# Kernel tuning notes

Hardware: AMD Instinct MI355X
Metric: run time of the kernel (lower is better)

The kernel has to match this reference:

```python
import jax, jax.numpy as jnp
import numpy as np

T, H, I, E, K = 1024, 1024, 512, 32, 4   # tokens, hidden, moe_inter, n_experts, top_k
G, TG, NS = 8, 4, 2                      # n_group, topk_group, n_shared_experts
C = 2 * T * K // E                       # expert capacity (no-drop headroom)
SCALE = 2.5                              # routed_scaling_factor


def setup_inputs() -> dict:
    key = jax.random.key(0)
    ks = jax.random.split(key, 7)
    s = 0.02
    return dict(
        hidden_states=jax.random.normal(ks[0], (T, H), jnp.float32),
        gate_w=jax.random.normal(ks[1], (E, H), jnp.float32) * s,
        e_bias=jax.random.normal(ks[2], (E,), jnp.float32) * 0.1,
        w_gate_up=jax.random.normal(ks[3], (E, 2 * I, H), jnp.float32) * s,
        w_down=jax.random.normal(ks[4], (E, H, I), jnp.float32) * s,
        w_gate_up_shared=jax.random.normal(ks[5], (2 * I * NS, H), jnp.float32) * s,
        w_down_shared=jax.random.normal(ks[6], (H, I * NS), jnp.float32) * s,
    )


def reference(hidden_states, gate_w, e_bias, w_gate_up, w_down, w_gate_up_shared, w_down_shared):
    x = hidden_states                                   # (T, H)
    # --- gate + sigmoid scoring (noaux_tc) ---
    logits = x @ gate_w.T                               # (T, E)
    scores = jax.nn.sigmoid(logits.astype(jnp.float32))
    sfc = scores + e_bias                               # scores_for_choice
    # --- group-limited top-k: top-2 sum per group, keep topk_group groups ---
    group_scores = jax.lax.top_k(sfc.reshape(T, G, E // G), 2)[0].sum(-1)  # (T, G)
    grp_idx = jax.lax.top_k(group_scores, TG)[1]        # (T, TG)
    gmask = jnp.zeros((T, G), jnp.float32).at[jnp.arange(T)[:, None], grp_idx].set(1.0)
    smask = jnp.repeat(gmask, E // G, axis=1)           # (T, E)
    sfc_m = jnp.where(smask > 0, sfc, 0.0)
    topk_idx = jax.lax.top_k(sfc_m, K)[1]               # (T, K)
    tw = jnp.take_along_axis(scores, topk_idx, axis=1)  # weights from raw scores
    tw = tw / (tw.sum(-1, keepdims=True) + 1e-20)       # norm_topk_prob
    tw = tw * SCALE
    # --- capacity-based dispatch (position within expert via cumsum of one-hot) ---
    e_flat = topk_idx.reshape(-1)                       # (T*K,)
    oh = jax.nn.one_hot(e_flat, E, dtype=jnp.float32)   # (T*K, E)
    pos = jnp.sum((jnp.cumsum(oh, axis=0) - 1.0) * oh, axis=-1).astype(jnp.int32)
    keep = (pos < C).astype(jnp.float32)                # capacity sized to never drop
    pos_c = jnp.clip(pos, 0, C - 1)
    t_flat = jnp.repeat(jnp.arange(T), K)
    combine = jnp.zeros((T, E, C), jnp.float32).at[t_flat, e_flat, pos_c].add(tw.reshape(-1) * keep)
    dispatch = jnp.zeros((T, E, C), jnp.float32).at[t_flat, e_flat, pos_c].add(keep)
    # --- grouped expert MLP (gate_up -> SiluAndMul -> down) ---
    xe = jnp.einsum('tec,th->ech', dispatch, x)         # (E, C, H)
    gu = jnp.einsum('ech,eoh->eco', xe, w_gate_up)      # (E, C, 2I)
    act = jax.nn.silu(gu[..., :I]) * gu[..., I:]
    ye = jnp.einsum('eci,ehi->ech', act, w_down)        # (E, C, H)
    routed = jnp.einsum('tec,ech->th', combine, ye)     # (T, H)
    # --- shared experts MLP on residual ---
    IS = I * NS
    gus = x @ w_gate_up_shared.T                        # (T, 2*IS)
    acts = jax.nn.silu(gus[:, :IS]) * gus[:, IS:]
    shared = acts @ w_down_shared.T                     # (T, H)
    return routed + shared
```

## Files before the change

### kernel.cpp

```cpp
#include <hip/hip_runtime.h>
#include <hip/hip_bf16.h>
#include <math.h>

#define T_TOK 1024
#define H_DIM 1024
#define I_DIM 512
#define E_NUM 32
#define K_TOP 4
#define G_NUM 8
#define TG_NUM 4
#define CAP 256
#define IS_DIM 1024
#define RSCALE 2.5f

#define WS_EIDX_OFF   1024
#define WS_WN_OFF     17408
#define WS_STOK_OFF   33792
#define WS_SW_OFF     66560
#define WS_ACT_OFF    99328
#define WS_ACTS_OFF   (99328 + (size_t)E_NUM*CAP*I_DIM*2)

typedef __attribute__((ext_vector_type(8))) short short8v;
typedef __attribute__((ext_vector_type(4))) short short4v;
typedef __attribute__((ext_vector_type(4))) float f32x4;

__device__ __forceinline__ short f2bf(float f) {
    unsigned u = __float_as_uint(f);
    u += 0x7FFFu + ((u >> 16) & 1u);
    return (short)(u >> 16);
}
__device__ __forceinline__ float silu_(float g) { return g / (1.f + expf(-g)); }

#define LDSTRIDE 40

__global__ __launch_bounds__(256) void gate_kernel(
    const float* __restrict__ x, const float* __restrict__ gate_w,
    const float* __restrict__ e_bias,
    int* __restrict__ eidx, float* __restrict__ wnorm)
{
    __shared__ float xs[H_DIM];
    __shared__ float logits[E_NUM];
    const int t = blockIdx.x;
    const int tid = threadIdx.x;
    ((float4*)xs)[tid] = ((const float4*)(x + (size_t)t * H_DIM))[tid];
    __syncthreads();

    const int e = tid >> 3, sub = tid & 7;
    const float* gw = gate_w + (size_t)e * H_DIM + sub * 128;
    const float* xr = xs + sub * 128;
    float p = 0.f;
    #pragma unroll 8
    for (int h = 0; h < 128; ++h) p += xr[h] * gw[h];
    for (int off = 4; off; off >>= 1) p += __shfl_down(p, off, 8);
    if (sub == 0) logits[e] = p;
    __syncthreads();
    if (tid != 0) return;

    float sc[E_NUM], sfc[E_NUM];
    for (int i = 0; i < E_NUM; ++i) {
        sc[i] = 1.f / (1.f + expf(-logits[i]));
        sfc[i] = sc[i] + e_bias[i];
    }
    float gs[G_NUM];
    for (int g = 0; g < G_NUM; ++g) {
        float m1 = -1e30f, m2 = -1e30f;
        for (int j = 0; j < E_NUM / G_NUM; ++j) {
            float v = sfc[g * (E_NUM / G_NUM) + j];
            if (v > m1) { m2 = m1; m1 = v; } else if (v > m2) m2 = v;
        }
        gs[g] = m1 + m2;
    }
    bool gm[G_NUM];
    for (int g = 0; g < G_NUM; ++g) gm[g] = false;
    for (int it = 0; it < TG_NUM; ++it) {
        int best = -1; float bv = -1e30f;
        for (int g = 0; g < G_NUM; ++g) if (!gm[g] && gs[g] > bv) { bv = gs[g]; best = g; }
        gm[best] = true;
    }
    float sm[E_NUM];
    for (int i = 0; i < E_NUM; ++i) sm[i] = gm[i / (E_NUM / G_NUM)] ? sfc[i] : 0.0f;
    int idx[K_TOP]; float w[K_TOP]; float tsum = 0.f;
    for (int it = 0; it < K_TOP; ++it) {
        int best = 0; float bv = -1e30f;
        for (int i = 0; i < E_NUM; ++i) if (sm[i] > bv) { bv = sm[i]; best = i; }
        sm[best] = -1e30f;
        idx[it] = best; w[it] = sc[best]; tsum += w[it];
    }
    float inv = RSCALE / (tsum + 1e-20f);
    const int base = t * K_TOP;
    for (int it = 0; it < K_TOP; ++it) {
        eidx[base + it] = idx[it];
        wnorm[base + it] = w[it] * inv;
    }
}

__global__ __launch_bounds__(256) void assign_kernel(
    const int* __restrict__ eidx, const float* __restrict__ wnorm,
    int* __restrict__ cnt, int* __restrict__ slot_token, float* __restrict__ slot_w)
{
    __shared__ int   se[T_TOK * K_TOP];
    __shared__ float swt[T_TOK * K_TOP];
    const int tid = threadIdx.x;
    for (int i = tid; i < T_TOK * K_TOP; i += 256) { se[i] = eidx[i]; swt[i] = wnorm[i]; }
    __syncthreads();

    const int e = tid >> 3;
    const int seg = tid & 7;
    const int base = seg * 512;
    int c = 0;
    for (int i = 0; i < 512; ++i) c += (se[base + i] == e);
    int excl = 0, total = 0;
    for (int s = 0; s < 8; ++s) {
        int cs = __shfl(c, s, 8);
        total += cs;
        if (s < seg) excl += cs;
    }
    if (seg == 0) cnt[e] = total;
    int pos = excl;
    for (int i = 0; i < 512; ++i) {
        if (se[base + i] == e) {
            if (pos < CAP) {
                slot_token[e * CAP + pos] = (base + i) >> 2;
                slot_w[e * CAP + pos] = swt[base + i];
            }
            ++pos;
        }
    }
}

#define WAVE_SETUP() \
    const int tid = threadIdx.x; const int lane = tid & 63; const int wid = tid >> 6; \
    const int wm = wid & 1, wn = wid >> 1; \
    const int lr16 = lane & 15, kc = lane >> 4; \
    const int kq = tid & 7; const int rbase = tid >> 3;

#define DECL_ACC() f32x4 acc[4][4]; \
    _Pragma("unroll") for (int i_ = 0; i_ < 4; ++i_) \
    _Pragma("unroll") for (int j_ = 0; j_ < 4; ++j_) acc[i_][j_] = 0.f;

#define STAGE_F32(dstoff, src, valid) do { \
    float4 v_ = (valid) ? *(const float4*)(src) : make_float4(0.f,0.f,0.f,0.f); \
    short4v sv_; sv_.x = f2bf(v_.x); sv_.y = f2bf(v_.y); sv_.z = f2bf(v_.z); sv_.w = f2bf(v_.w); \
    *(short4v*)(dstoff) = sv_; } while (0)

#define COMPUTE32() do { \
    short8v a_[4], b_[4]; \
    _Pragma("unroll") for (int mt = 0; mt < 4; ++mt) \
        a_[mt] = *(const short8v*)&As[(wm*64 + mt*16 + lr16)*LDSTRIDE + kc*8]; \
    _Pragma("unroll") for (int nt = 0; nt < 4; ++nt) \
        b_[nt] = *(const short8v*)&Bs[(wn*64 + nt*16 + lr16)*LDSTRIDE + kc*8]; \
    _Pragma("unroll") for (int mt = 0; mt < 4; ++mt) \
    _Pragma("unroll") for (int nt = 0; nt < 4; ++nt) \
        acc[mt][nt] = __builtin_amdgcn_mfma_f32_16x16x32_bf16(a_[mt], b_[nt], acc[mt][nt], 0, 0, 0); \
} while (0)

__global__ __launch_bounds__(256) void moe_gu_kernel(
    const float* __restrict__ x, const float* __restrict__ w_gate_up,
    const int* __restrict__ cnt, const int* __restrict__ slot_token,
    const float* __restrict__ slot_w, short* __restrict__ act)
{
    const int e = blockIdx.z;
    const int ne = min(cnt[e], CAP);
    const int r0 = blockIdx.y * 128;
    if (r0 >= ne) return;
    const int nI0 = blockIdx.x * 64;

    __shared__ __align__(16) short As[128 * LDSTRIDE];
    __shared__ __align__(16) short Bs[128 * LDSTRIDE];
    __shared__ int   toks[128];
    __shared__ float sws[128];

    WAVE_SETUP();
    if (tid < 128) {
        int p = r0 + tid;
        toks[tid] = (p < ne) ? slot_token[e * CAP + p] : 0;
        sws[tid]  = (p < ne) ? slot_w[e * CAP + p] : 0.f;
    }
    __syncthreads();

    const float* aptr[4]; bool aval[4]; int aoff[4];
    const float* bptr[4]; int boff[4];
    const float* wgu_e = w_gate_up + (size_t)e * (2 * I_DIM) * H_DIM;
    #pragma unroll
    for (int i = 0; i < 4; ++i) {
        int r = rbase + i * 32;
        aval[i] = (r0 + r) < ne;
        aptr[i] = x + (size_t)toks[r] * H_DIM + kq * 4;
        aoff[i] = r * LDSTRIDE + kq * 4;
        int c = r;
        int wrow = ((c >> 4) & 1) * I_DIM + nI0 + (c >> 5) * 16 + (c & 15);
        bptr[i] = wgu_e + (size_t)wrow * H_DIM + kq * 4;
        boff[i] = aoff[i];
    }

    DECL_ACC();
    for (int k0 = 0; k0 < H_DIM; k0 += 32) {
        #pragma unroll
        for (int i = 0; i < 4; ++i) STAGE_F32(&As[aoff[i]], aptr[i] + k0, aval[i]);
        #pragma unroll
        for (int i = 0; i < 4; ++i) STAGE_F32(&Bs[boff[i]], bptr[i] + k0, true);
        __syncthreads();
        COMPUTE32();
        __syncthreads();
    }

    #pragma unroll
    for (int mt = 0; mt < 4; ++mt) {
        #pragma unroll
        for (int q = 0; q < 2; ++q) {
            f32x4 g = acc[mt][2 * q], u = acc[mt][2 * q + 1];
            int colI = nI0 + (wn * 2 + q) * 16 + lr16;
            #pragma unroll
            for (int i = 0; i < 4; ++i) {
                int rl = wm * 64 + mt * 16 + kc * 4 + i;
                int p = r0 + rl;
                if (p < ne) {
                    float s = sws[rl];
                    float v = s * silu_(g[i]) * u[i];
                    act[((size_t)e * CAP + p) * I_DIM + colI] = f2bf(v);
                }
            }
        }
    }
}

__global__ __launch_bounds__(256) void moe_down_kernel(
    const short* __restrict__ act, const float* __restrict__ w_down,
    const int* __restrict__ cnt, const int* __restrict__ slot_token,
    float* __restrict__ out)
{
    const int e = blockIdx.z;
    const int ne = min(cnt[e], CAP);
    const int r0 = blockIdx.y * 128;
    if (r0 >= ne) return;
    const int h0 = blockIdx.x * 128;

    __shared__ __align__(16) short As[128 * LDSTRIDE];
    __shared__ __align__(16) short Bs[128 * LDSTRIDE];
    __shared__ int toks[128];

    WAVE_SETUP();
    if (tid < 128) {
        int p = r0 + tid;
        toks[tid] = (p < ne) ? slot_token[e * CAP + p] : 0;
    }
    __syncthreads();

    const short* aptr[4]; bool aval[4]; int aoff[4];
    const float* bptr[4];
    const float* wd_e = w_down + (size_t)e * H_DIM * I_DIM;
    #pragma unroll
    for (int i = 0; i < 4; ++i) {
        int r = rbase + i * 32;
        aval[i] = (r0 + r) < ne;
        aptr[i] = act + ((size_t)e * CAP + r0 + r) * I_DIM + kq * 4;
        aoff[i] = r * LDSTRIDE + kq * 4;
        bptr[i] = wd_e + (size_t)(h0 + r) * I_DIM + kq * 4;
    }

    DECL_ACC();
    for (int k0 = 0; k0 < I_DIM; k0 += 32) {
        #pragma unroll
        for (int i = 0; i < 4; ++i) {
            short4v sv = aval[i] ? *(const short4v*)(aptr[i] + k0) : (short4v)(short)0;
            *(short4v*)&As[aoff[i]] = sv;
        }
        #pragma unroll
        for (int i = 0; i < 4; ++i) STAGE_F32(&Bs[aoff[i]], bptr[i] + k0, true);
        __syncthreads();
        COMPUTE32();
        __syncthreads();
    }

    #pragma unroll
    for (int mt = 0; mt < 4; ++mt) {
        #pragma unroll
        for (int i = 0; i < 4; ++i) {
            int rl = wm * 64 + mt * 16 + kc * 4 + i;
            int p = r0 + rl;
            if (p < ne) {
                int tt = toks[rl];
                float* orow = out + (size_t)tt * H_DIM + h0 + wn * 64;
                #pragma unroll
                for (int nt = 0; nt < 4; ++nt)
                    atomicAdd(&orow[nt * 16 + lr16], acc[mt][nt][i]);
            }
        }
    }
}

__global__ __launch_bounds__(256) void shared_gu_kernel(
    const float* __restrict__ x, const float* __restrict__ w_gus,
    short* __restrict__ acts)
{
    const int t0 = blockIdx.y * 128;
    const int nI0 = blockIdx.x * 64;
    __shared__ __align__(16) short As[128 * LDSTRIDE];
    __shared__ __align__(16) short Bs[128 * LDSTRIDE];

    WAVE_SETUP();
    const float* aptr[4]; const float* bptr[4]; int aoff[4];
    #pragma unroll
    for (int i = 0; i < 4; ++i) {
        int r = rbase + i * 32;
        aptr[i] = x + (size_t)(t0 + r) * H_DIM + kq * 4;
        aoff[i] = r * LDSTRIDE + kq * 4;
        int c = r;
        int wrow = ((c >> 4) & 1) * IS_DIM + nI0 + (c >> 5) * 16 + (c & 15);
        bptr[i] = w_gus + (size_t)wrow * H_DIM + kq * 4;
    }

    DECL_ACC();
    for (int k0 = 0; k0 < H_DIM; k0 += 32) {
        #pragma unroll
        for (int i = 0; i < 4; ++i) STAGE_F32(&As[aoff[i]], aptr[i] + k0, true);
        #pragma unroll
        for (int i = 0; i < 4; ++i) STAGE_F32(&Bs[aoff[i]], bptr[i] + k0, true);
        __syncthreads();
        COMPUTE32();
        __syncthreads();
    }

    #pragma unroll
    for (int mt = 0; mt < 4; ++mt) {
        #pragma unroll
        for (int q = 0; q < 2; ++q) {
            f32x4 g = acc[mt][2 * q], u = acc[mt][2 * q + 1];
            int colI = nI0 + (wn * 2 + q) * 16 + lr16;
            #pragma unroll
            for (int i = 0; i < 4; ++i) {
                int t = t0 + wm * 64 + mt * 16 + kc * 4 + i;
                acts[(size_t)t * IS_DIM + colI] = f2bf(silu_(g[i]) * u[i]);
            }
        }
    }
}

__global__ __launch_bounds__(256) void shared_down_kernel(
    const short* __restrict__ acts, const float* __restrict__ w_ds,
    float* __restrict__ out)
{
    const int t0 = blockIdx.y * 128;
    const int h0 = blockIdx.x * 128;
    __shared__ __align__(16) short As[128 * LDSTRIDE];
    __shared__ __align__(16) short Bs[128 * LDSTRIDE];

    WAVE_SETUP();
    const short* aptr[4]; const float* bptr[4]; int aoff[4];
    #pragma unroll
    for (int i = 0; i < 4; ++i) {
        int r = rbase + i * 32;
        aptr[i] = acts + (size_t)(t0 + r) * IS_DIM + kq * 4;
        aoff[i] = r * LDSTRIDE + kq * 4;
        bptr[i] = w_ds + (size_t)(h0 + r) * IS_DIM + kq * 4;
    }

    DECL_ACC();
    for (int k0 = 0; k0 < IS_DIM; k0 += 32) {
        #pragma unroll
        for (int i = 0; i < 4; ++i) {
            short4v sv = *(const short4v*)(aptr[i] + k0);
            *(short4v*)&As[aoff[i]] = sv;
        }
        #pragma unroll
        for (int i = 0; i < 4; ++i) STAGE_F32(&Bs[aoff[i]], bptr[i] + k0, true);
        __syncthreads();
        COMPUTE32();
        __syncthreads();
    }

    #pragma unroll
    for (int mt = 0; mt < 4; ++mt) {
        #pragma unroll
        for (int i = 0; i < 4; ++i) {
            int t = t0 + wm * 64 + mt * 16 + kc * 4 + i;
            float* orow = out + (size_t)t * H_DIM + h0 + wn * 64;
            #pragma unroll
            for (int nt = 0; nt < 4; ++nt)
                orow[nt * 16 + lr16] = acc[mt][nt][i];
        }
    }
}

extern "C" void kernel_launch(void* const* d_in, const int* in_sizes, int n_in,
                              void* d_out, int out_size, void* d_ws, size_t ws_size,
                              hipStream_t stream) {
    const float* x   = (const float*)d_in[0];
    const float* gw  = (const float*)d_in[1];
    const float* eb  = (const float*)d_in[2];
    const float* wgu = (const float*)d_in[3];
    const float* wd  = (const float*)d_in[4];
    const float* wgs = (const float*)d_in[5];
    const float* wds = (const float*)d_in[6];
    float* out = (float*)d_out;
    char* ws = (char*)d_ws;

    int*   cnt   = (int*)(ws + 0);
    int*   eidx  = (int*)(ws + WS_EIDX_OFF);
    float* wnorm = (float*)(ws + WS_WN_OFF);
    int*   stok  = (int*)(ws + WS_STOK_OFF);
    float* sw    = (float*)(ws + WS_SW_OFF);
    short* act   = (short*)(ws + WS_ACT_OFF);
    short* acts  = (short*)(ws + WS_ACTS_OFF);

    gate_kernel<<<T_TOK, 256, 0, stream>>>(x, gw, eb, eidx, wnorm);
    assign_kernel<<<1, 256, 0, stream>>>(eidx, wnorm, cnt, stok, sw);
    shared_gu_kernel<<<dim3(IS_DIM / 64, T_TOK / 128), 256, 0, stream>>>(x, wgs, acts);
    shared_down_kernel<<<dim3(H_DIM / 128, T_TOK / 128), 256, 0, stream>>>(acts, wds, out);
    moe_gu_kernel<<<dim3(I_DIM / 64, CAP / 128, E_NUM), 256, 0, stream>>>(x, wgu, cnt, stok, sw, act);
    moe_down_kernel<<<dim3(H_DIM / 128, CAP / 128, E_NUM), 256, 0, stream>>>(act, wd, cnt, stok, out);
}
```

Baseline: 492.2 us.

## Use compact 64-row expert tile list with register-prefetched k-loop GEMMs

The assign kernel now builds a compact list of (expert, row-offset) tiles of 64 rows. The MoE GEMMs launch over this list instead of a fixed expert×capacity grid, which cuts the blocks that exit early and the padded rows in partly filled tiles. All four GEMM kernels move to 64×128 block tiles with launch_bounds occupancy hints. They also prefetch the next k-slice from global memory into registers while the current one is computed. FP32-to-bf16 conversion is packed with a byte-permute that rounds half-up rather than to nearest even, and the gate dot product is vectorised with float4. Smaller tiles give each block less reuse, and the rounding change shifts numerics slightly.

```diff
diff --git a/kernel.cpp b/kernel.cpp
--- a/kernel.cpp
+++ b/kernel.cpp
@@ -13,21 +13,33 @@
 #define IS_DIM 1024
 #define RSCALE 2.5f
 
-#define WS_EIDX_OFF   1024
-#define WS_WN_OFF     17408
-#define WS_STOK_OFF   33792
-#define WS_SW_OFF     66560
-#define WS_ACT_OFF    99328
-#define WS_ACTS_OFF   (99328 + (size_t)E_NUM*CAP*I_DIM*2)
+#define WS_CNT_OFF    0
+#define WS_NT_OFF     128
+#define WS_TILE_OFF   256
+#define WS_EIDX_OFF   4096
+#define WS_WN_OFF     20480
+#define WS_STOK_OFF   36864
+#define WS_SW_OFF     69632
+#define WS_ACT_OFF    102400
+#define WS_ACTS_OFF   (102400 + (size_t)E_NUM*CAP*I_DIM*2)
 
 typedef __attribute__((ext_vector_type(8))) short short8v;
-typedef __attribute__((ext_vector_type(4))) short short4v;
 typedef __attribute__((ext_vector_type(4))) float f32x4;
+typedef __attribute__((ext_vector_type(4))) unsigned uint4v;
 
 __device__ __forceinline__ short f2bf(float f) {
     unsigned u = __float_as_uint(f);
     u += 0x7FFFu + ((u >> 16) & 1u);
     return (short)(u >> 16);
+}
+__device__ __forceinline__ unsigned pk2bf(float a, float b) {
+    unsigned ua = __float_as_uint(a) + 0x8000u;
+    unsigned ub = __float_as_uint(b) + 0x8000u;
+    return __builtin_amdgcn_perm(ub, ua, 0x07060302);
+}
+__device__ __forceinline__ uint4v pk8bf(float4 lo, float4 hi) {
+    uint4v r; r.x = pk2bf(lo.x, lo.y); r.y = pk2bf(lo.z, lo.w);
+    r.z = pk2bf(hi.x, hi.y); r.w = pk2bf(hi.z, hi.w); return r;
 }
 __device__ __forceinline__ float silu_(float g) { return g / (1.f + expf(-g)); }
 
@@ -46,11 +58,14 @@
     __syncthreads();
 
     const int e = tid >> 3, sub = tid & 7;
-    const float* gw = gate_w + (size_t)e * H_DIM + sub * 128;
-    const float* xr = xs + sub * 128;
+    const float4* gw4 = (const float4*)(gate_w + (size_t)e * H_DIM + sub * 128);
+    const float4* xr4 = (const float4*)(xs + sub * 128);
     float p = 0.f;
-    #pragma unroll 8
-    for (int h = 0; h < 128; ++h) p += xr[h] * gw[h];
+    #pragma unroll
+    for (int h = 0; h < 32; ++h) {
+        float4 a = xr4[h], b = gw4[h];
+        p += a.x * b.x + a.y * b.y + a.z * b.z + a.w * b.w;
+    }
     for (int off = 4; off; off >>= 1) p += __shfl_down(p, off, 8);
     if (sub == 0) logits[e] = p;
     __syncthreads();
@@ -96,10 +111,12 @@
 
 __global__ __launch_bounds__(256) void assign_kernel(
     const int* __restrict__ eidx, const float* __restrict__ wnorm,
-    int* __restrict__ cnt, int* __restrict__ slot_token, float* __restrict__ slot_w)
+    int* __restrict__ cnt, int* __restrict__ slot_token, float* __restrict__ slot_w,
+    int* __restrict__ ntiles, int* __restrict__ tiles)
 {
     __shared__ int   se[T_TOK * K_TOP];
     __shared__ float swt[T_TOK * K_TOP];
+    __shared__ int   scnt[E_NUM];
     const int tid = threadIdx.x;
     for (int i = tid; i < T_TOK * K_TOP; i += 256) { se[i] = eidx[i]; swt[i] = wnorm[i]; }
     __syncthreads();
@@ -115,7 +132,7 @@
         total += cs;
         if (s < seg) excl += cs;
     }
-    if (seg == 0) cnt[e] = total;
+    if (seg == 0) { cnt[e] = total; scnt[e] = total; }
     int pos = excl;
     for (int i = 0; i < 512; ++i) {
         if (se[base + i] == e) {
@@ -126,161 +143,177 @@
             ++pos;
         }
     }
+    __syncthreads();
+    if (tid == 0) {
+        int nt = 0;
+        for (int ee = 0; ee < E_NUM; ++ee) {
+            int n = min(scnt[ee], CAP);
+            for (int r = 0; r < n; r += 64) {
+                tiles[nt * 4] = ee; tiles[nt * 4 + 1] = r; tiles[nt * 4 + 2] = n;
+                ++nt;
+            }
+        }
+        *ntiles = nt;
+    }
 }
 
 #define WAVE_SETUP() \
     const int tid = threadIdx.x; const int lane = tid & 63; const int wid = tid >> 6; \
     const int wm = wid & 1, wn = wid >> 1; \
     const int lr16 = lane & 15, kc = lane >> 4; \
-    const int kq = tid & 7; const int rbase = tid >> 3;
-
-#define DECL_ACC() f32x4 acc[4][4]; \
-    _Pragma("unroll") for (int i_ = 0; i_ < 4; ++i_) \
+    const int sc_ = tid & 3, srow = tid >> 2;
+
+#define DECL_ACC() f32x4 acc[2][4]; \
+    _Pragma("unroll") for (int i_ = 0; i_ < 2; ++i_) \
     _Pragma("unroll") for (int j_ = 0; j_ < 4; ++j_) acc[i_][j_] = 0.f;
 
-#define STAGE_F32(dstoff, src, valid) do { \
-    float4 v_ = (valid) ? *(const float4*)(src) : make_float4(0.f,0.f,0.f,0.f); \
-    short4v sv_; sv_.x = f2bf(v_.x); sv_.y = f2bf(v_.y); sv_.z = f2bf(v_.z); sv_.w = f2bf(v_.w); \
-    *(short4v*)(dstoff) = sv_; } while (0)
-
-#define COMPUTE32() do { \
-    short8v a_[4], b_[4]; \
-    _Pragma("unroll") for (int mt = 0; mt < 4; ++mt) \
-        a_[mt] = *(const short8v*)&As[(wm*64 + mt*16 + lr16)*LDSTRIDE + kc*8]; \
+#define COMPUTE_2x4() do { \
+    short8v a_[2], b_[4]; \
+    _Pragma("unroll") for (int mt = 0; mt < 2; ++mt) \
+        a_[mt] = *(const short8v*)&As[(wm*32 + mt*16 + lr16)*LDSTRIDE + kc*8]; \
     _Pragma("unroll") for (int nt = 0; nt < 4; ++nt) \
         b_[nt] = *(const short8v*)&Bs[(wn*64 + nt*16 + lr16)*LDSTRIDE + kc*8]; \
-    _Pragma("unroll") for (int mt = 0; mt < 4; ++mt) \
+    _Pragma("unroll") for (int mt = 0; mt < 2; ++mt) \
     _Pragma("unroll") for (int nt = 0; nt < 4; ++nt) \
         acc[mt][nt] = __builtin_amdgcn_mfma_f32_16x16x32_bf16(a_[mt], b_[nt], acc[mt][nt], 0, 0, 0); \
 } while (0)
 
-__global__ __launch_bounds__(256) void moe_gu_kernel(
+__global__ __launch_bounds__(256, 4) void moe_gu_kernel(
     const float* __restrict__ x, const float* __restrict__ w_gate_up,
-    const int* __restrict__ cnt, const int* __restrict__ slot_token,
-    const float* __restrict__ slot_w, short* __restrict__ act)
-{
-    const int e = blockIdx.z;
-    const int ne = min(cnt[e], CAP);
-    const int r0 = blockIdx.y * 128;
-    if (r0 >= ne) return;
+    const int* __restrict__ ntiles, const int* __restrict__ tiles,
+    const int* __restrict__ slot_token, const float* __restrict__ slot_w,
+    short* __restrict__ act)
+{
+    if ((int)blockIdx.y >= *ntiles) return;
+    const int e  = tiles[blockIdx.y * 4];
+    const int r0 = tiles[blockIdx.y * 4 + 1];
+    const int ne = tiles[blockIdx.y * 4 + 2];
     const int nI0 = blockIdx.x * 64;
 
-    __shared__ __align__(16) short As[128 * LDSTRIDE];
+    __shared__ __align__(16) short As[64 * LDSTRIDE];
     __shared__ __align__(16) short Bs[128 * LDSTRIDE];
-    __shared__ int   toks[128];
-    __shared__ float sws[128];
+    __shared__ int   toks[64];
+    __shared__ float sws[64];
 
     WAVE_SETUP();
-    if (tid < 128) {
-        int p = r0 + tid;
-        toks[tid] = (p < ne) ? slot_token[e * CAP + p] : 0;
-        sws[tid]  = (p < ne) ? slot_w[e * CAP + p] : 0.f;
-    }
-    __syncthreads();
-
-    const float* aptr[4]; bool aval[4]; int aoff[4];
-    const float* bptr[4]; int boff[4];
+    if (tid < 64) {
+        int p = r0 + tid; bool v = p < ne;
+        toks[tid] = v ? slot_token[e * CAP + p] : 0;
+        sws[tid]  = v ? slot_w[e * CAP + p] : 0.f;
+    }
+    __syncthreads();
+
+    const float* aptr = x + (size_t)toks[srow] * H_DIM + sc_ * 8;
     const float* wgu_e = w_gate_up + (size_t)e * (2 * I_DIM) * H_DIM;
+    const int cB1 = srow + 64;
+    const int wr0 = ((srow >> 4) & 1) * I_DIM + nI0 + ((srow >> 5) << 4) + (srow & 15);
+    const int wr1 = ((cB1 >> 4) & 1) * I_DIM + nI0 + ((cB1 >> 5) << 4) + (cB1 & 15);
+    const float* bptr0 = wgu_e + (size_t)wr0 * H_DIM + sc_ * 8;
+    const float* bptr1 = wgu_e + (size_t)wr1 * H_DIM + sc_ * 8;
+    const int aoff = srow * LDSTRIDE + sc_ * 8;
+    const int boff0 = srow * LDSTRIDE + sc_ * 8;
+    const int boff1 = cB1 * LDSTRIDE + sc_ * 8;
+
+    DECL_ACC();
+    float4 cA0 = *(const float4*)(aptr), cA1 = *(const float4*)(aptr + 4);
+    float4 cB0a = *(const float4*)(bptr0), cB0b = *(const float4*)(bptr0 + 4);
+    float4 cB1a = *(const float4*)(bptr1), cB1b = *(const float4*)(bptr1 + 4);
+
+    for (int k0 = 0; k0 < H_DIM; k0 += 32) {
+        float4 nA0, nA1, nB0a, nB0b, nB1a, nB1b;
+        const int k1 = k0 + 32;
+        if (k1 < H_DIM) {
+            nA0 = *(const float4*)(aptr + k1);  nA1 = *(const float4*)(aptr + k1 + 4);
+            nB0a = *(const float4*)(bptr0 + k1); nB0b = *(const float4*)(bptr0 + k1 + 4);
+            nB1a = *(const float4*)(bptr1 + k1); nB1b = *(const float4*)(bptr1 + k1 + 4);
+        }
+        *(uint4v*)&As[aoff]  = pk8bf(cA0, cA1);
+        *(uint4v*)&Bs[boff0] = pk8bf(cB0a, cB0b);
+        *(uint4v*)&Bs[boff1] = pk8bf(cB1a, cB1b);
+        __syncthreads();
+        COMPUTE_2x4();
+        __syncthreads();
+        cA0 = nA0; cA1 = nA1; cB0a = nB0a; cB0b = nB0b; cB1a = nB1a; cB1b = nB1b;
+    }
+
     #pragma unroll
-    for (int i = 0; i < 4; ++i) {
-        int r = rbase + i * 32;
-        aval[i] = (r0 + r) < ne;
-        aptr[i] = x + (size_t)toks[r] * H_DIM + kq * 4;
-        aoff[i] = r * LDSTRIDE + kq * 4;
-        int c = r;
-        int wrow = ((c >> 4) & 1) * I_DIM + nI0 + (c >> 5) * 16 + (c & 15);
-        bptr[i] = wgu_e + (size_t)wrow * H_DIM + kq * 4;
-        boff[i] = aoff[i];
-    }
-
-    DECL_ACC();
-    for (int k0 = 0; k0 < H_DIM; k0 += 32) {
-        #pragma unroll
-        for (int i = 0; i < 4; ++i) STAGE_F32(&As[aoff[i]], aptr[i] + k0, aval[i]);
-        #pragma unroll
-        for (int i = 0; i < 4; ++i) STAGE_F32(&Bs[boff[i]], bptr[i] + k0, true);
-        __syncthreads();
-        COMPUTE32();
-        __syncthreads();
-    }
-
-    #pragma unroll
-    for (int mt = 0; mt < 4; ++mt) {
+    for (int mt = 0; mt < 2; ++mt) {
         #pragma unroll
         for (int q = 0; q < 2; ++q) {
             f32x4 g = acc[mt][2 * q], u = acc[mt][2 * q + 1];
-            int colI = nI0 + (wn * 2 + q) * 16 + lr16;
+            int colI = nI0 + wn * 32 + q * 16 + lr16;
             #pragma unroll
             for (int i = 0; i < 4; ++i) {
-                int rl = wm * 64 + mt * 16 + kc * 4 + i;
+                int rl = wm * 32 + mt * 16 + kc * 4 + i;
                 int p = r0 + rl;
                 if (p < ne) {
                     float s = sws[rl];
-                    float v = s * silu_(g[i]) * u[i];
-                    act[((size_t)e * CAP + p) * I_DIM + colI] = f2bf(v);
+                    act[((size_t)e * CAP + p) * I_DIM + colI] = f2bf(s * silu_(g[i]) * u[i]);
                 }
             }
         }
     }
 }
 
-__global__ __launch_bounds__(256) void moe_down_kernel(
+__global__ __launch_bounds__(256, 4) void moe_down_kernel(
     const short* __restrict__ act, const float* __restrict__ w_down,
-    const int* __restrict__ cnt, const int* __restrict__ slot_token,
-    float* __restrict__ out)
-{
-    const int e = blockIdx.z;
-    const int ne = min(cnt[e], CAP);
-    const int r0 = blockIdx.y * 128;
-    if (r0 >= ne) return;
+    const int* __restrict__ ntiles, const int* __restrict__ tiles,
+    const int* __restrict__ slot_token, float* __restrict__ out)
+{
+    if ((int)blockIdx.y >= *ntiles) return;
+    const int e  = tiles[blockIdx.y * 4];
+    const int r0 = tiles[blockIdx.y * 4 + 1];
+    const int ne = tiles[blockIdx.y * 4 + 2];
     const int h0 = blockIdx.x * 128;
 
-    __shared__ __align__(16) short As[128 * LDSTRIDE];
+    __shared__ __align__(16) short As[64 * LDSTRIDE];
     __shared__ __align__(16) short Bs[128 * LDSTRIDE];
-    __shared__ int toks[128];
+    __shared__ int toks[64];
 
     WAVE_SETUP();
-    if (tid < 128) {
+    if (tid < 64) {
         int p = r0 + tid;
         toks[tid] = (p < ne) ? slot_token[e * CAP + p] : 0;
     }
     __syncthreads();
 
-    const short* aptr[4]; bool aval[4]; int aoff[4];
-    const float* bptr[4];
+    const short* aptr = act + ((size_t)e * CAP + r0 + srow) * I_DIM + sc_ * 8;
     const float* wd_e = w_down + (size_t)e * H_DIM * I_DIM;
+    const float* bptr0 = wd_e + (size_t)(h0 + srow) * I_DIM + sc_ * 8;
+    const float* bptr1 = wd_e + (size_t)(h0 + srow + 64) * I_DIM + sc_ * 8;
+    const int aoff = srow * LDSTRIDE + sc_ * 8;
+    const int boff1 = (srow + 64) * LDSTRIDE + sc_ * 8;
+
+    DECL_ACC();
+    short8v cA = *(const short8v*)(aptr);
+    float4 cB0a = *(const float4*)(bptr0), cB0b = *(const float4*)(bptr0 + 4);
+    float4 cB1a = *(const float4*)(bptr1), cB1b = *(const float4*)(bptr1 + 4);
+
+    for (int k0 = 0; k0 < I_DIM; k0 += 32) {
+        short8v nA; float4 nB0a, nB0b, nB1a, nB1b;
+        const int k1 = k0 + 32;
+        if (k1 < I_DIM) {
+            nA = *(const short8v*)(aptr + k1);
+            nB0a = *(const float4*)(bptr0 + k1); nB0b = *(const float4*)(bptr0 + k1 + 4);
+            nB1a = *(const float4*)(bptr1 + k1); nB1b = *(const float4*)(bptr1 + k1 + 4);
+        }
+        *(short8v*)&As[aoff] = cA;
+        *(uint4v*)&Bs[aoff]  = pk8bf(cB0a, cB0b);
+        *(uint4v*)&Bs[boff1] = pk8bf(cB1a, cB1b);
+        __syncthreads();
+        COMPUTE_2x4();
+        __syncthreads();
+        cA = nA; cB0a = nB0a; cB0b = nB0b; cB1a = nB1a; cB1b = nB1b;
+    }
+
     #pragma unroll
-    for (int i = 0; i < 4; ++i) {
-        int r = rbase + i * 32;
-        aval[i] = (r0 + r) < ne;
-        aptr[i] = act + ((size_t)e * CAP + r0 + r) * I_DIM + kq * 4;
-        aoff[i] = r * LDSTRIDE + kq * 4;
-        bptr[i] = wd_e + (size_t)(h0 + r) * I_DIM + kq * 4;
-    }
-
-    DECL_ACC();
-    for (int k0 = 0; k0 < I_DIM; k0 += 32) {
+    for (int mt = 0; mt < 2; ++mt) {
         #pragma unroll
         for (int i = 0; i < 4; ++i) {
-            short4v sv = aval[i] ? *(const short4v*)(aptr[i] + k0) : (short4v)(short)0;
-            *(short4v*)&As[aoff[i]] = sv;
-        }
-        #pragma unroll
-        for (int i = 0; i < 4; ++i) STAGE_F32(&Bs[aoff[i]], bptr[i] + k0, true);
-        __syncthreads();
-        COMPUTE32();
-        __syncthreads();
-    }
-
-    #pragma unroll
-    for (int mt = 0; mt < 4; ++mt) {
-        #pragma unroll
-        for (int i = 0; i < 4; ++i) {
-            int rl = wm * 64 + mt * 16 + kc * 4 + i;
+            int rl = wm * 32 + mt * 16 + kc * 4 + i;
             int p = r0 + rl;
             if (p < ne) {
-                int tt = toks[rl];
-                float* orow = out + (size_t)tt * H_DIM + h0 + wn * 64;
+                float* orow = out + (size_t)toks[rl] * H_DIM + h0 + wn * 64;
                 #pragma unroll
                 for (int nt = 0; nt < 4; ++nt)
                     atomicAdd(&orow[nt * 16 + lr16], acc[mt][nt][i]);
@@ -289,91 +322,105 @@
     }
 }
 
-__global__ __launch_bounds__(256) void shared_gu_kernel(
+__global__ __launch_bounds__(256, 4) void shared_gu_kernel(
     const float* __restrict__ x, const float* __restrict__ w_gus,
     short* __restrict__ acts)
 {
-    const int t0 = blockIdx.y * 128;
+    const int t0 = blockIdx.y * 64;
     const int nI0 = blockIdx.x * 64;
-    __shared__ __align__(16) short As[128 * LDSTRIDE];
+    __shared__ __align__(16) short As[64 * LDSTRIDE];
     __shared__ __align__(16) short Bs[128 * LDSTRIDE];
 
     WAVE_SETUP();
-    const float* aptr[4]; const float* bptr[4]; int aoff[4];
+    const float* aptr = x + (size_t)(t0 + srow) * H_DIM + sc_ * 8;
+    const int cB1 = srow + 64;
+    const int wr0 = ((srow >> 4) & 1) * IS_DIM + nI0 + ((srow >> 5) << 4) + (srow & 15);
+    const int wr1 = ((cB1 >> 4) & 1) * IS_DIM + nI0 + ((cB1 >> 5) << 4) + (cB1 & 15);
+    const float* bptr0 = w_gus + (size_t)wr0 * H_DIM + sc_ * 8;
+    const float* bptr1 = w_gus + (size_t)wr1 * H_DIM + sc_ * 8;
+    const int aoff = srow * LDSTRIDE + sc_ * 8;
+    const int boff1 = cB1 * LDSTRIDE + sc_ * 8;
+
+    DECL_ACC();
+    float4 cA0 = *(const float4*)(aptr), cA1 = *(const float4*)(aptr + 4);
+    float4 cB0a = *(const float4*)(bptr0), cB0b = *(const float4*)(bptr0 + 4);
+    float4 cB1a = *(const float4*)(bptr1), cB1b = *(const float4*)(bptr1 + 4);
+
+    for (int k0 = 0; k0 < H_DIM; k0 += 32) {
+        float4 nA0, nA1, nB0a, nB0b, nB1a, nB1b;
+        const int k1 = k0 + 32;
+        if (k1 < H_DIM) {
+            nA0 = *(const float4*)(aptr + k1);  nA1 = *(const float4*)(aptr + k1 + 4);
+            nB0a = *(const float4*)(bptr0 + k1); nB0b = *(const float4*)(bptr0 + k1 + 4);
+            nB1a = *(const float4*)(bptr1 + k1); nB1b = *(const float4*)(bptr1 + k1 + 4);
+        }
+        *(uint4v*)&As[aoff]  = pk8bf(cA0, cA1);
+        *(uint4v*)&Bs[aoff]  = pk8bf(cB0a, cB0b);
+        *(uint4v*)&Bs[boff1] = pk8bf(cB1a, cB1b);
+        __syncthreads();
+        COMPUTE_2x4();
+        __syncthreads();
+        cA0 = nA0; cA1 = nA1; cB0a = nB0a; cB0b = nB0b; cB1a = nB1a; cB1b = nB1b;
+    }
+
     #pragma unroll
-    for (int i = 0; i < 4; ++i) {
-        int r = rbase + i * 32;
-        aptr[i] = x + (size_t)(t0 + r) * H_DIM + kq * 4;
-        aoff[i] = r * LDSTRIDE + kq * 4;
-        int c = r;
-        int wrow = ((c >> 4) & 1) * IS_DIM + nI0 + (c >> 5) * 16 + (c & 15);
-        bptr[i] = w_gus + (size_t)wrow * H_DIM + kq * 4;
-    }
-
-    DECL_ACC();
-    for (int k0 = 0; k0 < H_DIM; k0 += 32) {
-        #pragma unroll
-        for (int i = 0; i < 4; ++i) STAGE_F32(&As[aoff[i]], aptr[i] + k0, true);
-        #pragma unroll
-        for (int i = 0; i < 4; ++i) STAGE_F32(&Bs[aoff[i]], bptr[i] + k0, true);
-        __syncthreads();
-        COMPUTE32();
-        __syncthreads();
-    }
-
-    #pragma unroll
-    for (int mt = 0; mt < 4; ++mt) {
+    for (int mt = 0; mt < 2; ++mt) {
         #pragma unroll
         for (int q = 0; q < 2; ++q) {
             f32x4 g = acc[mt][2 * q], u = acc[mt][2 * q + 1];
-            int colI = nI0 + (wn * 2 + q) * 16 + lr16;
+            int colI = nI0 + wn * 32 + q * 16 + lr16;
             #pragma unroll
             for (int i = 0; i < 4; ++i) {
-                int t = t0 + wm * 64 + mt * 16 + kc * 4 + i;
+                int t = t0 + wm * 32 + mt * 16 + kc * 4 + i;
                 acts[(size_t)t * IS_DIM + colI] = f2bf(silu_(g[i]) * u[i]);
             }
         }
     }
 }
 
-__global__ __launch_bounds__(256) void shared_down_kernel(
+__global__ __launch_bounds__(256, 4) void shared_down_kernel(
     const short* __restrict__ acts, const float* __restrict__ w_ds,
     float* __restrict__ out)
 {
-    const int t0 = blockIdx.y * 128;
+    const int t0 = blockIdx.y * 64;
     const int h0 = blockIdx.x * 128;
-    __shared__ __align__(16) short As[128 * LDSTRIDE];
+    __shared__ __align__(16) short As[64 * LDSTRIDE];
     __shared__ __align__(16) short Bs[128 * LDSTRIDE];
 
     WAVE_SETUP();
-    const short* aptr[4]; const float* bptr[4]; int aoff[4];
+    const short* aptr = acts + (size_t)(t0 + srow) * IS_DIM + sc_ * 8;
+    const float* bptr0 = w_ds + (size_t)(h0 + srow) * IS_DIM + sc_ * 8;
+    const float* bptr1 = w_ds + (size_t)(h0 + srow + 64) * IS_DIM + sc_ * 8;
+    const int aoff = srow * LDSTRIDE + sc_ * 8;
+    const int boff1 = (srow + 64) * LDSTRIDE + sc_ * 8;
+
+    DECL_ACC();
+    short8v cA = *(const short8v*)(aptr);
+    float4 cB0a = *(const float4*)(bptr0), cB0b = *(const float4*)(bptr0 + 4);
+    float4 cB1a = *(const float4*)(bptr1), cB1b = *(const float4*)(bptr1 + 4);
+
+    for (int k0 = 0; k0 < IS_DIM; k0 += 32) {
+        short8v nA; float4 nB0a, nB0b, nB1a, nB1b;
+        const int k1 = k0 + 32;
+        if (k1 < IS_DIM) {
+            nA = *(const short8v*)(aptr + k1);
+            nB0a = *(const float4*)(bptr0 + k1); nB0b = *(const float4*)(bptr0 + k1 + 4);
+            nB1a = *(const float4*)(bptr1 + k1); nB1b = *(const float4*)(bptr1 + k1 + 4);
+        }
+        *(short8v*)&As[aoff] = cA;
+        *(uint4v*)&Bs[aoff]  = pk8bf(cB0a, cB0b);
+        *(uint4v*)&Bs[boff1] = pk8bf(cB1a, cB1b);
+        __syncthreads();
+        COMPUTE_2x4();
+        __syncthreads();
+        cA = nA; cB0a = nB0a; cB0b = nB0b; cB1a = nB1a; cB1b = nB1b;
+    }
+
     #pragma unroll
-    for (int i = 0; i < 4; ++i) {
-        int r = rbase + i * 32;
-        aptr[i] = acts + (size_t)(t0 + r) * IS_DIM + kq * 4;
-        aoff[i] = r * LDSTRIDE + kq * 4;
-        bptr[i] = w_ds + (size_t)(h0 + r) * IS_DIM + kq * 4;
-    }
-
-    DECL_ACC();
-    for (int k0 = 0; k0 < IS_DIM; k0 += 32) {
+    for (int mt = 0; mt < 2; ++mt) {
         #pragma unroll
         for (int i = 0; i < 4; ++i) {
-            short4v sv = *(const short4v*)(aptr[i] + k0);
-            *(short4v*)&As[aoff[i]] = sv;
-        }
-        #pragma unroll
-        for (int i = 0; i < 4; ++i) STAGE_F32(&Bs[aoff[i]], bptr[i] + k0, true);
-        __syncthreads();
-        COMPUTE32();
-        __syncthreads();
-    }
-
-    #pragma unroll
-    for (int mt = 0; mt < 4; ++mt) {
-        #pragma unroll
-        for (int i = 0; i < 4; ++i) {
-            int t = t0 + wm * 64 + mt * 16 + kc * 4 + i;
+            int t = t0 + wm * 32 + mt * 16 + kc * 4 + i;
             float* orow = out + (size_t)t * H_DIM + h0 + wn * 64;
             #pragma unroll
             for (int nt = 0; nt < 4; ++nt)
@@ -395,18 +442,20 @@
     float* out = (float*)d_out;
     char* ws = (char*)d_ws;
 
-    int*   cnt   = (int*)(ws + 0);
-    int*   eidx  = (int*)(ws + WS_EIDX_OFF);
-    float* wnorm = (float*)(ws + WS_WN_OFF);
-    int*   stok  = (int*)(ws + WS_STOK_OFF);
-    float* sw    = (float*)(ws + WS_SW_OFF);
-    short* act   = (short*)(ws + WS_ACT_OFF);
-    short* acts  = (short*)(ws + WS_ACTS_OFF);
+    int*   cnt    = (int*)(ws + WS_CNT_OFF);
+    int*   ntiles = (int*)(ws + WS_NT_OFF);
+    int*   tiles  = (int*)(ws + WS_TILE_OFF);
+    int*   eidx   = (int*)(ws + WS_EIDX_OFF);
+    float* wnorm  = (float*)(ws + WS_WN_OFF);
+    int*   stok   = (int*)(ws + WS_STOK_OFF);
+    float* sw     = (float*)(ws + WS_SW_OFF);
+    short* act    = (short*)(ws + WS_ACT_OFF);
+    short* acts   = (short*)(ws + WS_ACTS_OFF);
 
     gate_kernel<<<T_TOK, 256, 0, stream>>>(x, gw, eb, eidx, wnorm);
-    assign_kernel<<<1, 256, 0, stream>>>(eidx, wnorm, cnt, stok, sw);
-    shared_gu_kernel<<<dim3(IS_DIM / 64, T_TOK / 128), 256, 0, stream>>>(x, wgs, acts);
-    shared_down_kernel<<<dim3(H_DIM / 128, T_TOK / 128), 256, 0, stream>>>(acts, wds, out);
-    moe_gu_kernel<<<dim3(I_DIM / 64, CAP / 128, E_NUM), 256, 0, stream>>>(x, wgu, cnt, stok, sw, act);
-    moe_down_kernel<<<dim3(H_DIM / 128, CAP / 128, E_NUM), 256, 0, stream>>>(act, wd, cnt, stok, out);
-}
+    assign_kernel<<<1, 256, 0, stream>>>(eidx, wnorm, cnt, stok, sw, ntiles, tiles);
+    shared_gu_kernel<<<dim3(IS_DIM / 64, T_TOK / 64), 256, 0, stream>>>(x, wgs, acts);
+    shared_down_kernel<<<dim3(H_DIM / 128, T_TOK / 64), 256, 0, stream>>>(acts, wds, out);
+    moe_gu_kernel<<<dim3(I_DIM / 64, 128), 256, 0, stream>>>(x, wgu, ntiles, tiles, stok, sw, act);
+    moe_down_kernel<<<dim3(H_DIM / 128, 128), 256, 0, stream>>>(act, wd, ntiles, tiles, stok, out);
+}
```

Result: faster. 432.0 us (-12.2%).
